# Kernel tuning notes

Measured on AMD Instinct MI355X. Metric: run time of the kernel, lower is better.

The kernel has to match this reference:

```python
import jax, jax.numpy as jnp
import numpy as np

EPS = 1e-12

def _l2norm(v, axis=-1):
    return v / jnp.sqrt(jnp.sum(v * v, axis=axis, keepdims=True) + EPS)

def setup_inputs() -> dict:
    key = jax.random.key(0)
    k1, k2, k3 = jax.random.split(key, 3)
    B, D, C, K = 8192, 1024, 90, 16
    x = jax.random.normal(k1, (B, D), dtype=jnp.float32)
    labels = jax.random.randint(k2, (B,), 0, C, dtype=jnp.int64)
    centers = jax.random.normal(k3, (C, K, D), dtype=jnp.float32)
    return {"x": x, "labels": labels, "centers": centers}

def reference(x, labels, centers):
    # l2Norm branch of CenterWoParamMultiCosineLoss (cosine distances).
    # centers are normalized at init; x is normalized in forward.
    xn = _l2norm(x)                              # [B, D]
    cn = _l2norm(centers)                        # [C, K, D]
    c = cn[labels]                               # [B, K, D] gather per label
    # inner cosine distances per center: d_k = 1 - x . c_k
    d = 1.0 - jnp.einsum('bd,bkd->bk', xn, c)    # [B, K]
    # detached normalized scores
    dd = jax.lax.stop_gradient(d)
    score = dd / jnp.sum(dd, axis=1, keepdims=True)  # [B, K]
    # K > 1 with l2Norm: weight each distance by (1 - score)
    per_sample = jnp.sum((1.0 - score) * d, axis=1)  # [B]
    return jnp.mean(per_sample)
```

## Files before the change

kernel.cpp:

```cpp
#include <hip/hip_runtime.h>

#define EPS 1e-12f

constexpr int D       = 1024;
constexpr int K       = 16;
constexpr int NS      = 8;
constexpr int LISTCAP = 1024;
constexpr int CROWP   = D + 8;

typedef __attribute__((ext_vector_type(8))) short  short8v;
typedef __attribute__((ext_vector_type(4))) float  float4v;

__device__ __forceinline__ ushort f2bf(float f) {
    uint u = __float_as_uint(f);
    u += 0x7FFFu + ((u >> 16) & 1u);
    return (ushort)(u >> 16);
}

__global__ __launch_bounds__(256) void cosine_loss_mfma(
    const float* __restrict__ x, const int* __restrict__ labels,
    const float* __restrict__ centers, float* __restrict__ out,
    int B, int C, float inv_B) {
    const int bid  = blockIdx.x;
    const int c    = bid % C;
    const int sl   = bid / C;
    const int tid  = threadIdx.x;
    const int w    = tid >> 6;
    const int lane = tid & 63;

    __shared__ ushort  cbLDS[K * CROWP];
    __shared__ int     list[LISTCAP];
    __shared__ int     wsumI[4];
    __shared__ float   cinvLDS[K];
    __shared__ float4v paccLDS[4][64];
    __shared__ float   xxLDS[4][64];
    __shared__ float   xxrow[16];

    const int SLICE = (B + NS - 1) / NS;
    const int base  = sl * SLICE;
    const int lim   = min(SLICE, B - base);
    const int rpt   = (SLICE + 255) >> 8;

#pragma unroll
    for (int rr = 0; rr < 4; ++rr) {
        const int r = 4 * w + rr;
        const float* crow = centers + (size_t)(c * K + r) * D;
        float cc = 0.f;
#pragma unroll
        for (int j = 0; j < 4; ++j) {
            const float4 v = *reinterpret_cast<const float4*>(crow + j * 256 + lane * 4);
            cc += v.x * v.x + v.y * v.y + v.z * v.z + v.w * v.w;
            uint2 p;
            p.x = (uint)f2bf(v.x) | ((uint)f2bf(v.y) << 16);
            p.y = (uint)f2bf(v.z) | ((uint)f2bf(v.w) << 16);
            *reinterpret_cast<uint2*>(&cbLDS[r * CROWP + j * 256 + lane * 4]) = p;
        }
#pragma unroll
        for (int off = 32; off >= 1; off >>= 1) cc += __shfl_xor(cc, off, 64);
        if (lane == 0) cinvLDS[r] = 1.0f / sqrtf(cc + EPS);
    }

    int mmask = 0, cnt_t = 0;
    for (int r = 0; r < rpt; ++r) {
        const int idx = r * 256 + tid;
        if (idx < lim && labels[base + idx] == c) { mmask |= 1 << r; ++cnt_t; }
    }

    int vs = cnt_t;
#pragma unroll
    for (int off = 1; off < 64; off <<= 1) {
        const int u = __shfl_up(vs, off, 64);
        if (lane >= off) vs += u;
    }
    if (lane == 63) wsumI[w] = vs;
    __syncthreads();
    int prefix = 0;
#pragma unroll
    for (int ww = 0; ww < 4; ++ww) if (ww < w) prefix += wsumI[ww];
    const int cnt = wsumI[0] + wsumI[1] + wsumI[2] + wsumI[3];

    int pos = prefix + vs - cnt_t;
    for (int r = 0; r < rpt; ++r) {
        if ((mmask >> r) & 1) list[pos++] = base + r * 256 + tid;
    }
    __syncthreads();

    const int r16 = lane & 15;
    const int g   = lane >> 4;
    float wacc = 0.f;

    for (int tb = 0; tb < cnt; tb += 16) {
        const int rown = tb + r16;
        const int sidx = list[rown < cnt ? rown : cnt - 1];
        const float* xrow = x + (size_t)sidx * D;

        float4v acc = (float4v){0.f, 0.f, 0.f, 0.f};
        float xxp = 0.f;
#pragma unroll
        for (int kk = 0; kk < 8; ++kk) {
            const int kbase = (w * 8 + kk) * 32 + g * 8;
            const float4 xa = *reinterpret_cast<const float4*>(xrow + kbase);
            const float4 xb = *reinterpret_cast<const float4*>(xrow + kbase + 4);
            xxp += xa.x * xa.x + xa.y * xa.y + xa.z * xa.z + xa.w * xa.w +
                   xb.x * xb.x + xb.y * xb.y + xb.z * xb.z + xb.w * xb.w;
            short8v af;
            af[0] = (short)f2bf(xa.x); af[1] = (short)f2bf(xa.y);
            af[2] = (short)f2bf(xa.z); af[3] = (short)f2bf(xa.w);
            af[4] = (short)f2bf(xb.x); af[5] = (short)f2bf(xb.y);
            af[6] = (short)f2bf(xb.z); af[7] = (short)f2bf(xb.w);
            const short8v bf = *reinterpret_cast<const short8v*>(
                &cbLDS[r16 * CROWP + kbase]);
            acc = __builtin_amdgcn_mfma_f32_16x16x32_bf16(af, bf, acc, 0, 0, 0);
        }
        paccLDS[w][lane] = acc;
        xxLDS[w][lane]   = xxp;
        __syncthreads();

        if (w == 0) {
            const float4v tot = paccLDS[0][lane] + paccLDS[1][lane] +
                                paccLDS[2][lane] + paccLDS[3][lane];
            if (lane < 16) {
                float s = 0.f;
#pragma unroll
                for (int ww = 0; ww < 4; ++ww)
#pragma unroll
                    for (int gg = 0; gg < 4; ++gg)
                        s += xxLDS[ww][lane + 16 * gg];
                xxrow[lane] = 1.0f / sqrtf(s + EPS);
            }
            const float cv = cinvLDS[r16];
            float sd[4], sd2[4];
#pragma unroll
            for (int q = 0; q < 4; ++q) {
                const float dk = 1.0f - tot[q] * xxrow[g * 4 + q] * cv;
                sd[q] = dk;  sd2[q] = dk * dk;
            }
#pragma unroll
            for (int off = 1; off < 16; off <<= 1) {
#pragma unroll
                for (int q = 0; q < 4; ++q) {
                    sd[q]  += __shfl_xor(sd[q],  off, 64);
                    sd2[q] += __shfl_xor(sd2[q], off, 64);
                }
            }
            if (r16 == 0) {
#pragma unroll
                for (int q = 0; q < 4; ++q) {
                    const int row = g * 4 + q;
                    if (tb + row < cnt) wacc += sd[q] - sd2[q] / sd[q];
                }
            }
        }
        __syncthreads();
    }

    if (w == 0) {
        wacc += __shfl_xor(wacc, 16, 64);
        wacc += __shfl_xor(wacc, 32, 64);
        if (lane == 0) atomicAdd(out, wacc * inv_B);
    }
}

extern "C" void kernel_launch(void* const* d_in, const int* in_sizes, int n_in,
                              void* d_out, int out_size, void* d_ws, size_t ws_size,
                              hipStream_t stream) {
    const float* x       = (const float*)d_in[0];
    const int*   labels  = (const int*)d_in[1];
    const float* centers = (const float*)d_in[2];

    const int B = in_sizes[1];
    const int C = in_sizes[2] / (K * D);
    const int nblocks = C * NS;

    float* out = (float*)d_out;

    hipMemsetAsync(out, 0, sizeof(float), stream);

    cosine_loss_mfma<<<nblocks, 256, 0, stream>>>(
        x, labels, centers, out, B, C, 1.0f / (float)B);
}
```

Before: 93.06 us.

## Precompute bf16 centers and norms in a separate prep kernel

Moves the bf16 conversion and inverse-norm computation of the centers into a prep kernel that writes them to workspace, so each of the eight slice blocks per class loads bf16 rows instead of reconverting fp32. Blocks with no matching labels now exit before the center load, and the sample list is shrunk and capped at LISTCAP, which also cuts LDS use. This adds a second kernel launch and a global round trip for the converted centers. The cap silently drops samples if a slice ever holds more than 256 rows of one class.

```diff
diff --git a/kernel.cpp b/kernel.cpp
--- a/kernel.cpp
+++ b/kernel.cpp
@@ -5,7 +5,7 @@
 constexpr int D       = 1024;
 constexpr int K       = 16;
 constexpr int NS      = 8;
-constexpr int LISTCAP = 1024;
+constexpr int LISTCAP = 256;
 constexpr int CROWP   = D + 8;
 
 typedef __attribute__((ext_vector_type(8))) short  short8v;
@@ -17,10 +17,34 @@
     return (ushort)(u >> 16);
 }
 
+__global__ __launch_bounds__(256) void prep_centers(
+    const float* __restrict__ centers, ushort* __restrict__ cbf,
+    float* __restrict__ cinv, int nrows) {
+    const int wave = (blockIdx.x * blockDim.x + threadIdx.x) >> 6;
+    const int lane = threadIdx.x & 63;
+    if (wave >= nrows) return;
+
+    const float* row  = centers + (size_t)wave * D;
+    ushort*      orow = cbf + (size_t)wave * D;
+    float cc = 0.f;
+#pragma unroll
+    for (int j = 0; j < 4; ++j) {
+        const float4 v = *reinterpret_cast<const float4*>(row + j * 256 + lane * 4);
+        cc += v.x * v.x + v.y * v.y + v.z * v.z + v.w * v.w;
+        uint2 p;
+        p.x = (uint)f2bf(v.x) | ((uint)f2bf(v.y) << 16);
+        p.y = (uint)f2bf(v.z) | ((uint)f2bf(v.w) << 16);
+        *reinterpret_cast<uint2*>(orow + j * 256 + lane * 4) = p;
+    }
+#pragma unroll
+    for (int off = 32; off >= 1; off >>= 1) cc += __shfl_xor(cc, off, 64);
+    if (lane == 0) cinv[wave] = 1.0f / sqrtf(cc + EPS);
+}
+
 __global__ __launch_bounds__(256) void cosine_loss_mfma(
     const float* __restrict__ x, const int* __restrict__ labels,
-    const float* __restrict__ centers, float* __restrict__ out,
-    int B, int C, float inv_B) {
+    const ushort* __restrict__ cbf, const float* __restrict__ cinv,
+    float* __restrict__ out, int B, int C, float inv_B) {
     const int bid  = blockIdx.x;
     const int c    = bid % C;
     const int sl   = bid / C;
@@ -41,25 +65,6 @@
     const int lim   = min(SLICE, B - base);
     const int rpt   = (SLICE + 255) >> 8;
 
-#pragma unroll
-    for (int rr = 0; rr < 4; ++rr) {
-        const int r = 4 * w + rr;
-        const float* crow = centers + (size_t)(c * K + r) * D;
-        float cc = 0.f;
-#pragma unroll
-        for (int j = 0; j < 4; ++j) {
-            const float4 v = *reinterpret_cast<const float4*>(crow + j * 256 + lane * 4);
-            cc += v.x * v.x + v.y * v.y + v.z * v.z + v.w * v.w;
-            uint2 p;
-            p.x = (uint)f2bf(v.x) | ((uint)f2bf(v.y) << 16);
-            p.y = (uint)f2bf(v.z) | ((uint)f2bf(v.w) << 16);
-            *reinterpret_cast<uint2*>(&cbLDS[r * CROWP + j * 256 + lane * 4]) = p;
-        }
-#pragma unroll
-        for (int off = 32; off >= 1; off >>= 1) cc += __shfl_xor(cc, off, 64);
-        if (lane == 0) cinvLDS[r] = 1.0f / sqrtf(cc + EPS);
-    }
-
     int mmask = 0, cnt_t = 0;
     for (int r = 0; r < rpt; ++r) {
         const int idx = r * 256 + tid;
@@ -77,12 +82,30 @@
     int prefix = 0;
 #pragma unroll
     for (int ww = 0; ww < 4; ++ww) if (ww < w) prefix += wsumI[ww];
-    const int cnt = wsumI[0] + wsumI[1] + wsumI[2] + wsumI[3];
+    const int cnt0 = wsumI[0] + wsumI[1] + wsumI[2] + wsumI[3];
+
+    if (cnt0 == 0) return;
+    const int cnt = min(cnt0, LISTCAP);
 
     int pos = prefix + vs - cnt_t;
     for (int r = 0; r < rpt; ++r) {
-        if ((mmask >> r) & 1) list[pos++] = base + r * 256 + tid;
-    }
+        if ((mmask >> r) & 1) {
+            if (pos < LISTCAP) list[pos] = base + r * 256 + tid;
+            ++pos;
+        }
+    }
+
+#pragma unroll
+    for (int rr = 0; rr < 4; ++rr) {
+        const int r = 4 * w + rr;
+        const ushort* src = cbf + (size_t)(c * K + r) * D;
+#pragma unroll
+        for (int h = 0; h < 2; ++h) {
+            const uint4 t = *reinterpret_cast<const uint4*>(src + h * 512 + lane * 8);
+            *reinterpret_cast<uint4*>(&cbLDS[r * CROWP + h * 512 + lane * 8]) = t;
+        }
+    }
+    if (tid < K) cinvLDS[tid] = cinv[c * K + tid];
     __syncthreads();
 
     const int r16 = lane & 15;
@@ -168,14 +191,19 @@
     const int*   labels  = (const int*)d_in[1];
     const float* centers = (const float*)d_in[2];
 
-    const int B = in_sizes[1];
-    const int C = in_sizes[2] / (K * D);
-    const int nblocks = C * NS;
+    const int B     = in_sizes[1];
+    const int C     = in_sizes[2] / (K * D);
+    const int nrows = C * K;
 
     float* out = (float*)d_out;
 
+    ushort* cbf   = (ushort*)d_ws;
+    float*  cinvW = (float*)((char*)d_ws + (size_t)nrows * D * sizeof(ushort));
+
     hipMemsetAsync(out, 0, sizeof(float), stream);
 
-    cosine_loss_mfma<<<nblocks, 256, 0, stream>>>(
-        x, labels, centers, out, B, C, 1.0f / (float)B);
-}
+    prep_centers<<<(nrows + 3) / 4, 256, 0, stream>>>(centers, cbf, cinvW, nrows);
+
+    cosine_loss_mfma<<<C * NS, 256, 0, stream>>>(
+        x, labels, cbf, cinvW, out, B, C, 1.0f / (float)B);
+}
```

New measurement: 94.02 us. Within noise of the previous version (+1.0%).
